# Optimization experiments

Measured on AMD Instinct MI355X. Metric: run time of the kernel, lower is better.

## Reference

```python
import jax, jax.numpy as jnp
import numpy as np

BLKQ = 64
BLKK = 64
TOPK_RATIO = 0.125


def setup_inputs() -> dict:
    key = jax.random.key(0)
    ks = jax.random.split(key, 4)
    B, L, H, D = 1, 4096, 16, 64
    q = jax.random.normal(ks[0], (B, L, H, D), jnp.float32)
    k = jax.random.normal(ks[1], (B, L, H, D), jnp.float32)
    v = jax.random.normal(ks[2], (B, L, H, D), jnp.float32)
    w_proj = jax.random.normal(ks[3], (D, D), jnp.float32) * 0.02
    b_proj = jnp.zeros((D,), jnp.float32)
    return {"q": q, "k": k, "v": v, "w_proj": w_proj, "b_proj": b_proj}


def _sparse_linear_attn(q, k, v, w_proj, b_proj):
    # q,k,v: (B, L, H, D) -> (B, H, L, D)
    q = jnp.transpose(q, (0, 2, 1, 3))
    k = jnp.transpose(k, (0, 2, 1, 3))
    v = jnp.transpose(v, (0, 2, 1, 3))
    B, H, L, D = q.shape
    M, N = L // BLKQ, L // BLKK  # L chosen divisible by block sizes (no padding)
    T = max(1, int(TOPK_RATIO * N))  # selected key blocks per query block

    qb = q.reshape(B, H, M, BLKQ, D)
    kb = k.reshape(B, H, N, BLKK, D)
    vb = v.reshape(B, H, N, BLKK, D)

    # --- block map: mean-pooled block descriptors, topk key blocks per query block ---
    qm = qb.mean(axis=3)  # (B,H,M,D)
    km = kb.mean(axis=3)  # (B,H,N,D)
    blk_scores = jnp.einsum('bhmd,bhnd->bhmn', qm, km)
    _, lut = jax.lax.top_k(blk_scores, T)  # (B,H,M,T) int32

    # --- gather selected K/V blocks ---
    b_idx = jnp.arange(B)[:, None, None, None]
    h_idx = jnp.arange(H)[None, :, None, None]
    k_sel = kb[b_idx, h_idx, lut]  # (B,H,M,T,BLKK,D)
    v_sel = vb[b_idx, h_idx, lut]  # (B,H,M,T,BLKK,D)

    # --- block-sparse softmax attention over gathered keys only ---
    scale = D ** (-0.5)
    att = jnp.einsum('bhmqd,bhmtkd->bhmqtk', qb, k_sel) * scale
    att = att.reshape(B, H, M, BLKQ, T * BLKK)
    p = jax.nn.softmax(att, axis=-1)
    o_s = jnp.einsum('bhmqn,bhmnd->bhmqd', p, v_sel.reshape(B, H, M, T * BLKK, D))
    o_s = o_s.reshape(B, H, L, D)

    # --- global linear attention with softmax feature map ---
    q_fm = jax.nn.softmax(q, axis=-1)
    k_fm = jax.nn.softmax(k, axis=-1)
    kvsum = jnp.einsum('bhld,bhle->bhde', k_fm, v)  # (B,H,D,D)
    ksum = k_fm.sum(axis=2)  # (B,H,D)
    num = jnp.einsum('bhld,bhde->bhle', q_fm, kvsum)
    den = jnp.einsum('bhld,bhd->bhl', q_fm, ksum)[..., None] + 1e-6
    o_l = num / den
    o_l = jnp.einsum('bhld,ed->bhle', o_l, w_proj) + b_proj  # nn.Linear: x @ W.T + b

    o = o_s + o_l
    return jnp.transpose(o, (0, 2, 1, 3))  # (B, L, H, D)


def reference(q, k, v, w_proj, b_proj):
    return _sparse_linear_attn(q, k, v, w_proj, b_proj)
```

## Files before the change

### kernel.cpp

```cpp
#include <hip/hip_runtime.h>


#define NH   16
#define DH   64
#define NBLK 64
#define TSEL 8

typedef unsigned short u16;
typedef unsigned int   u32;
typedef __attribute__((ext_vector_type(8))) short short8;
typedef __attribute__((ext_vector_type(4))) float f4;
typedef __attribute__((ext_vector_type(4))) u32 u32x4;

#define MFMA_BF16(a, b, c) __builtin_amdgcn_mfma_f32_16x16x32_bf16(a, b, c, 0, 0, 0)

__device__ __forceinline__ u16 f2bf_rne(float f) {
  u32 u = __float_as_uint(f);
  u += 0x7fffu + ((u >> 16) & 1u);
  return (u16)(u >> 16);
}
__device__ __forceinline__ u32 pk2(float a, float b) {
  return (u32)f2bf_rne(a) | ((u32)f2bf_rne(b) << 16);
}
__device__ __forceinline__ float bf2f(u16 u) { return __uint_as_float(((u32)u) << 16); }

__device__ __forceinline__ short8 frag_row(const u16* t, int row, int jblk) {
  return *(const short8*)((const char*)t + row * 128 + ((jblk ^ (row & 7)) * 16));
}

__device__ __forceinline__ void gload_lds16(const char* g, char* l) {
  __builtin_amdgcn_global_load_lds(
      (const __attribute__((address_space(1))) char*)g,
      (__attribute__((address_space(3))) char*)l, 16, 0, 0);
}

__device__ __forceinline__ void stage_async(const char* ktb, const char* vtb,
                                            char* dst, int w, int lane) {
  const char* s = ((w & 2) ? vtb : ktb) + (w & 1) * 4096 + lane * 16;
  char* d = dst + ((w & 2) ? 8192 : 0) + (w & 1) * 4096 + lane * 16;
#pragma unroll
  for (int i = 0; i < 4; i++) gload_lds16(s + i * 1024, d + i * 1024);
}

__device__ __forceinline__ void stage_m2(const char* m2b, const float* ksum_h,
                                         const float* bproj, char* dst,
                                         int w, int lane) {
  if (w < 2) {
    const char* s = m2b + w * 4096 + lane * 16;
    char* d = dst + w * 4096 + lane * 16;
#pragma unroll
    for (int i = 0; i < 4; i++) gload_lds16(s + i * 1024, d + i * 1024);
  } else if (w == 2 && lane < 32) {
    const char* s = (lane < 16) ? ((const char*)ksum_h + lane * 16)
                                : ((const char*)bproj + (lane - 16) * 16);
    gload_lds16(s, dst + 8192 + lane * 16);
  }
}

__global__ __launch_bounds__(256) void prep_kernel(const float* __restrict__ k,
                                                   const float* __restrict__ v,
                                                   u16* __restrict__ kT,
                                                   u16* __restrict__ vT,
                                                   float* __restrict__ kvp,
                                                   float* __restrict__ ksp,
                                                   float* __restrict__ kmv) {
  __shared__ __align__(16) char vsl[8192];
  __shared__ __align__(16) char kfm[8192];
  __shared__ float redmx[256];
  __shared__ float redsm[256];
  __shared__ float kmred[256];
  __shared__ float ksred[256];
  __shared__ float mxf[64];
  __shared__ float smi[64];
  int b = blockIdx.x;
  int n = (b >> 3) & 63;
  int h = 2 * (b & 7) + (b >> 9);
  int tid = threadIdx.x;
  int w = tid >> 6, lane = tid & 63;
  int row = lane, qd = w;
  int lq = lane & 15, quad = lane >> 4;

  float kv[16];
  {
    const float* kr = k + (size_t)(n * 64 + row) * 1024 + h * 64 + qd * 16;
#pragma unroll
    for (int c4 = 0; c4 < 4; c4++) {
      float4 a = *(const float4*)(kr + c4 * 4);
      kv[c4 * 4] = a.x; kv[c4 * 4 + 1] = a.y; kv[c4 * 4 + 2] = a.z; kv[c4 * 4 + 3] = a.w;
    }
  }
  {
    uint4 w0 = make_uint4(pk2(kv[0], kv[1]), pk2(kv[2], kv[3]),
                          pk2(kv[4], kv[5]), pk2(kv[6], kv[7]));
    uint4 w1 = make_uint4(pk2(kv[8], kv[9]), pk2(kv[10], kv[11]),
                          pk2(kv[12], kv[13]), pk2(kv[14], kv[15]));
    *(uint4*)(vsl + row * 128 + (((2 * qd) ^ (row & 7)) * 16)) = w0;
    *(uint4*)(vsl + row * 128 + (((2 * qd + 1) ^ (row & 7)) * 16)) = w1;
  }
  {
    float mx = kv[0];
#pragma unroll
    for (int j = 1; j < 16; j++) mx = fmaxf(mx, kv[j]);
    redmx[qd * 64 + row] = mx;
  }
  __syncthreads();

  {
    uint4* kt_out = (uint4*)(kT + ((size_t)(h * 64 + n)) * 4096);
    kt_out[tid] = ((const uint4*)vsl)[tid];
    kt_out[256 + tid] = ((const uint4*)vsl)[256 + tid];
  }
  {
    float mx = fmaxf(fmaxf(redmx[row], redmx[64 + row]),
                     fmaxf(redmx[128 + row], redmx[192 + row]));
    float sm = 0.f;
#pragma unroll
    for (int j = 0; j < 16; j++) sm += __expf(kv[j] - mx);
    redsm[qd * 64 + row] = sm;
  }
  __syncthreads();
  if (tid < 64) {
    mxf[tid] = fmaxf(fmaxf(redmx[tid], redmx[64 + tid]),
                     fmaxf(redmx[128 + tid], redmx[192 + tid]));
    smi[tid] = 1.0f / (redsm[tid] + redsm[64 + tid] + redsm[128 + tid] + redsm[192 + tid]);
  }
  __syncthreads();

  {
    int c = lane, g = w;
    const float* kcg = k + (size_t)(n * 64 + g * 16) * 1024 + h * 64 + c;
    float e[16];
    float pk = 0.f;
#pragma unroll
    for (int i = 0; i < 16; i++) {
      float x = kcg[(size_t)i * 1024];
      pk += x;
      int r = g * 16 + i;
      e[i] = __expf(x - mxf[r]) * smi[r];
    }
    kmred[g * 64 + c] = pk;
    uint4 x0 = make_uint4(pk2(e[0], e[1]), pk2(e[2], e[3]),
                          pk2(e[4], e[5]), pk2(e[6], e[7]));
    uint4 x1 = make_uint4(pk2(e[8], e[9]), pk2(e[10], e[11]),
                          pk2(e[12], e[13]), pk2(e[14], e[15]));
    *(uint4*)(kfm + c * 128 + (((2 * g) ^ (c & 7)) * 16)) = x0;
    *(uint4*)(kfm + c * 128 + (((2 * g + 1) ^ (c & 7)) * 16)) = x1;
  }
  {
    int c = lane, g = w;
    const float* vcol = v + (size_t)(n * 64 + g * 16) * 1024 + h * 64 + c;
    float vv[16];
#pragma unroll
    for (int i = 0; i < 16; i++) vv[i] = vcol[(size_t)i * 1024];
    uint4 x0 = make_uint4(pk2(vv[0], vv[1]), pk2(vv[2], vv[3]),
                          pk2(vv[4], vv[5]), pk2(vv[6], vv[7]));
    uint4 x1 = make_uint4(pk2(vv[8], vv[9]), pk2(vv[10], vv[11]),
                          pk2(vv[12], vv[13]), pk2(vv[14], vv[15]));
    *(uint4*)(vsl + c * 128 + (((2 * g) ^ (c & 7)) * 16)) = x0;
    *(uint4*)(vsl + c * 128 + (((2 * g + 1) ^ (c & 7)) * 16)) = x1;
  }
  __syncthreads();

  {
    uint4* vt_out = (uint4*)(vT + ((size_t)(h * 64 + n)) * 4096);
    vt_out[tid] = ((const uint4*)vsl)[tid];
    vt_out[256 + tid] = ((const uint4*)vsl)[256 + tid];
  }
  if (tid < 64)
    kmv[h * 4096 + n * 64 + tid] =
        (kmred[tid] + kmred[64 + tid] + kmred[128 + tid] + kmred[192 + tid]) * (1.0f / 64.0f);
  {
    float ks = 0.f;
    short8 x0 = frag_row((const u16*)kfm, lane, 2 * w);
    short8 x1 = frag_row((const u16*)kfm, lane, 2 * w + 1);
#pragma unroll
    for (int e = 0; e < 8; e++) ks += bf2f((u16)x0[e]) + bf2f((u16)x1[e]);
    ksred[tid] = ks;
  }
  {
    f4 acc[4];
    f4 zz = {0.f, 0.f, 0.f, 0.f};
#pragma unroll
    for (int et = 0; et < 4; et++) acc[et] = zz;
#pragma unroll
    for (int ks2 = 0; ks2 < 2; ks2++) {
      short8 a_ = frag_row((const u16*)kfm, w * 16 + lq, 4 * ks2 + quad);
#pragma unroll
      for (int et = 0; et < 4; et++)
        acc[et] = MFMA_BF16(a_, frag_row((const u16*)vsl, et * 16 + lq, 4 * ks2 + quad), acc[et]);
    }
    float* kvb = kvp + ((size_t)(h * 64 + n)) * 4096;
#pragma unroll
    for (int r = 0; r < 4; r++)
#pragma unroll
      for (int et = 0; et < 4; et++)
        kvb[(w * 16 + quad * 4 + r) * 64 + et * 16 + lq] = acc[et][r];
  }
  __syncthreads();
  if (tid < 64)
    ksp[((size_t)(h * 64 + n)) * 64 + tid] = ksred[tid] + ksred[64 + tid] +
                                             ksred[128 + tid] + ksred[192 + tid];
}

__global__ __launch_bounds__(256) void post_kernel(const float* __restrict__ kvp,
                                                   const float* __restrict__ ksp,
                                                   const float* __restrict__ wgt,
                                                   u16* __restrict__ m2t,
                                                   float* __restrict__ ksum) {
  __shared__ float kr[4][64];
  __shared__ float wl[64 * 65];
  int bx = blockIdx.x, tid = threadIdx.x;
  int h = bx >> 4, dq = bx & 15;
  int j = tid & 63, rr = tid >> 6;

  {
    size_t off = (size_t)(dq * 4 + rr) * 64 + j;
    const float* base = kvp + (size_t)h * 64 * 4096 + off;
    float s0 = 0.f, s1 = 0.f, s2 = 0.f, s3 = 0.f;
#pragma unroll
    for (int n4 = 0; n4 < 16; n4++) {
      s0 += base[(size_t)(n4 * 4 + 0) * 4096];
      s1 += base[(size_t)(n4 * 4 + 1) * 4096];
      s2 += base[(size_t)(n4 * 4 + 2) * 4096];
      s3 += base[(size_t)(n4 * 4 + 3) * 4096];
    }
    kr[rr][j] = (s0 + s1) + (s2 + s3);
  }
#pragma unroll
  for (int i = 0; i < 16; i++) {
    int f = i * 256 + tid;
    wl[(f >> 6) * 65 + (f & 63)] = wgt[f];
  }
  __syncthreads();

  {
    int e = tid & 63, rr2 = tid >> 6;
    float acc = 0.f;
#pragma unroll
    for (int jj = 0; jj < 64; jj++) acc = fmaf(kr[rr2][jj], wl[e * 65 + jj], acc);
    int d = dq * 4 + rr2;
    *(u16*)((char*)m2t + (size_t)h * 8192 + e * 128 +
            (((d >> 3) ^ (e & 7)) * 16) + (d & 7) * 2) = f2bf_rne(acc);
  }
  if (dq == 0 && tid < 64) {
    const float* base = ksp + (size_t)h * 64 * 64 + tid;
    float s = 0.f;
#pragma unroll
    for (int n = 0; n < 64; n++) s += base[(size_t)n * 64];
    ksum[h * 64 + tid] = s;
  }
}

__global__ __launch_bounds__(256, 4) void fused_attn_kernel(const float* __restrict__ q,
                                                            const u16* __restrict__ kT,
                                                            const u16* __restrict__ vT,
                                                            const float* __restrict__ kmv,
                                                            const u16* __restrict__ m2t,
                                                            const float* __restrict__ ksum,
                                                            const float* __restrict__ bproj,
                                                            float* __restrict__ out) {
  __shared__ __align__(16) char smem[40960];
  int b = blockIdx.x;
  int m = (b >> 3) & 63;
  int h = 2 * (b & 7) + (b >> 9);
  int tid = threadIdx.x, w = tid >> 6, lane = tid & 63;
  int lq = lane & 15, quad = lane >> 4;
  char* bufA = smem;
  char* bufB = smem + 16384;
  char* p_b = smem + 32768 + w * 2048;
  float* km_s = (float*)smem;
  float* qmp = (float*)(smem + 20480);
  float* qmf = (float*)(smem + 21504);

  {
    int c = tid & 63, g = tid >> 6;
    const float* qcol = q + ((size_t)(m * 64 + g * 16)) * 1024 + h * 64 + c;
    float qp = 0.f;
#pragma unroll
    for (int i = 0; i < 16; i++) qp += qcol[(size_t)i * 1024];
    qmp[g * 64 + c] = qp;
#pragma unroll
    for (int i = 0; i < 16; i++) {
      int idx = i * 256 + tid;
      km_s[(idx >> 6) * 65 + (idx & 63)] = kmv[h * 4096 + idx];
    }
  }
  __syncthreads();
  if (tid < 64) qmf[tid] = qmp[tid] + qmp[64 + tid] + qmp[128 + tid] + qmp[192 + tid];
  __syncthreads();
  int blks[8];
  {
    int n = lane;
    float s = 0.f;
#pragma unroll
    for (int d = 0; d < 64; d++) s += qmf[d] * km_s[n * 65 + d];
    float my = s;
#pragma unroll
    for (int t = 0; t < TSEL; t++) {
      float vv = my; int idx = n;
#pragma unroll
      for (int off = 1; off < 64; off <<= 1) {
        float ov = __shfl_xor(vv, off);
        int oi = __shfl_xor(idx, off);
        if (ov > vv || (ov == vv && oi < idx)) { vv = ov; idx = oi; }
      }
      int sel = __builtin_amdgcn_readfirstlane(idx);
      blks[t] = sel;
      if (n == sel) my = -INFINITY;
    }
  }
  __syncthreads();

  const int qrow = w * 16 + lq;
  const float* qr_g = q + ((size_t)(m * 64 + qrow)) * 1024 + h * 64;
  short8 qf[2];
#pragma unroll
  for (int ks = 0; ks < 2; ks++) {
    const float* gp = qr_g + (4 * ks + quad) * 8;
    float4 a = *(const float4*)gp;
    float4 bb = *(const float4*)(gp + 4);
    u32x4 tt = {pk2(a.x, a.y), pk2(a.z, a.w), pk2(bb.x, bb.y), pk2(bb.z, bb.w)};
    qf[ks] = __builtin_bit_cast(short8, tt);
  }

  stage_async((const char*)(kT + ((size_t)(h * 64 + blks[0])) * 4096),
              (const char*)(vT + ((size_t)(h * 64 + blks[0])) * 4096),
              bufA, w, lane);
  __syncthreads();

  float mrun = -INFINITY, lrun = 0.f;
  f4 o[4];
  f4 zz = {0.f, 0.f, 0.f, 0.f};
#pragma unroll
  for (int et = 0; et < 4; et++) o[et] = zz;

  char* cur = bufA;
  char* nxt = bufB;

  for (int t = 0; t < 8; t++) {
    if (t < 7)
      stage_async((const char*)(kT + ((size_t)(h * 64 + blks[t + 1])) * 4096),
                  (const char*)(vT + ((size_t)(h * 64 + blks[t + 1])) * 4096),
                  nxt, w, lane);
    else
      stage_m2((const char*)m2t + (size_t)h * 8192, ksum + h * 64, bproj,
               nxt, w, lane);

    const u16* kc = (const u16*)cur;
    const u16* vc = (const u16*)(cur + 8192);

    f4 s[4];
#pragma unroll
    for (int kt = 0; kt < 4; kt++) s[kt] = zz;
    __builtin_amdgcn_s_setprio(1);
#pragma unroll
    for (int ks = 0; ks < 2; ks++)
#pragma unroll
      for (int kt = 0; kt < 4; kt++)
        s[kt] = MFMA_BF16(frag_row(kc, kt * 16 + lq, 4 * ks + quad), qf[ks], s[kt]);
    __builtin_amdgcn_s_setprio(0);

    float mp = -INFINITY;
#pragma unroll
    for (int kt = 0; kt < 4; kt++)
#pragma unroll
      for (int r = 0; r < 4; r++) mp = fmaxf(mp, s[kt][r]);
    mp = fmaxf(mp, __shfl_xor(mp, 16));
    mp = fmaxf(mp, __shfl_xor(mp, 32));
    mp *= 0.125f;
    if (__any(mp > mrun)) {
      float mn = fmaxf(mrun, mp);
      float al = __expf(mrun - mn);
      mrun = mn;
      lrun *= al;
#pragma unroll
      for (int et = 0; et < 4; et++)
#pragma unroll
        for (int r = 0; r < 4; r++) o[et][r] *= al;
    }
    float rs_ = 0.f;
#pragma unroll
    for (int kt = 0; kt < 4; kt++) {
      float p0 = __expf(fmaf(s[kt][0], 0.125f, -mrun));
      float p1 = __expf(fmaf(s[kt][1], 0.125f, -mrun));
      float p2 = __expf(fmaf(s[kt][2], 0.125f, -mrun));
      float p3 = __expf(fmaf(s[kt][3], 0.125f, -mrun));
      rs_ += p0 + p1 + p2 + p3;
      u32 lo32 = (__float_as_uint(p0) >> 16) | (__float_as_uint(p1) & 0xffff0000u);
      u32 hi32 = (__float_as_uint(p2) >> 16) | (__float_as_uint(p3) & 0xffff0000u);
      int addr = lq * 128 + (((kt * 2 + (quad >> 1)) ^ (lq & 7)) * 16) + (quad & 1) * 8;
      *(uint2*)(p_b + addr) = make_uint2(lo32, hi32);
    }
    rs_ += __shfl_xor(rs_, 16);
    rs_ += __shfl_xor(rs_, 32);
    lrun += rs_;

    __builtin_amdgcn_s_setprio(1);
#pragma unroll
    for (int ks = 0; ks < 2; ks++) {
      short8 pf = frag_row((const u16*)p_b, lq, 4 * ks + quad);
#pragma unroll
      for (int et = 0; et < 4; et++)
        o[et] = MFMA_BF16(frag_row(vc, et * 16 + lq, 4 * ks + quad), pf, o[et]);
    }
    __builtin_amdgcn_s_setprio(0);

    __syncthreads();
    char* tmp = cur; cur = nxt; nxt = tmp;
  }

  u16* m2_l = (u16*)cur;
  float* ks_s = (float*)(cur + 8192);
  float* b_s = (float*)(cur + 8448);

  float ev[16];
  float mx = -INFINITY;
#pragma unroll
  for (int c4 = 0; c4 < 4; c4++) {
    float4 a = *(const float4*)(qr_g + quad * 16 + c4 * 4);
    ev[c4 * 4] = a.x; ev[c4 * 4 + 1] = a.y; ev[c4 * 4 + 2] = a.z; ev[c4 * 4 + 3] = a.w;
    mx = fmaxf(mx, fmaxf(fmaxf(a.x, a.y), fmaxf(a.z, a.w)));
  }
  mx = fmaxf(mx, __shfl_xor(mx, 16));
  mx = fmaxf(mx, __shfl_xor(mx, 32));
  float sum = 0.f, eks = 0.f;
#pragma unroll
  for (int j = 0; j < 16; j++) {
    float e = __expf(ev[j] - mx);
    ev[j] = e;
    sum += e;
    eks += e * ks_s[quad * 16 + j];
  }
  sum += __shfl_xor(sum, 16); sum += __shfl_xor(sum, 32);
  eks += __shfl_xor(eks, 16); eks += __shfl_xor(eks, 32);
  float invs = 1.0f / sum;
  float den = fmaf(eks, invs, 1e-6f);
  float scale = invs / den;
  uint4 e0v = make_uint4(pk2(ev[0], ev[1]), pk2(ev[2], ev[3]),
                         pk2(ev[4], ev[5]), pk2(ev[6], ev[7]));
  uint4 e1v = make_uint4(pk2(ev[8], ev[9]), pk2(ev[10], ev[11]),
                         pk2(ev[12], ev[13]), pk2(ev[14], ev[15]));
  *(uint4*)(p_b + lq * 128 + (((2 * quad) ^ (lq & 7)) * 16)) = e0v;
  *(uint4*)(p_b + lq * 128 + (((2 * quad + 1) ^ (lq & 7)) * 16)) = e1v;

  f4 oc[4];
  f4 zz2 = {0.f, 0.f, 0.f, 0.f};
#pragma unroll
  for (int et = 0; et < 4; et++) oc[et] = zz2;
  __builtin_amdgcn_s_setprio(1);
#pragma unroll
  for (int ks2 = 0; ks2 < 2; ks2++) {
    short8 ef = frag_row((const u16*)p_b, lq, 4 * ks2 + quad);
#pragma unroll
    for (int et = 0; et < 4; et++)
      oc[et] = MFMA_BF16(frag_row(m2_l, et * 16 + lq, 4 * ks2 + quad), ef, oc[et]);
  }
  __builtin_amdgcn_s_setprio(0);

  float invl = 1.0f / lrun;
  float* gp = out + ((size_t)(m * 64 + qrow)) * 1024 + h * 64 + quad * 4;
#pragma unroll
  for (int et = 0; et < 4; et++) {
    int e0 = et * 16 + quad * 4;
    float4 ov;
    ov.x = o[et][0] * invl + oc[et][0] * scale + b_s[e0 + 0];
    ov.y = o[et][1] * invl + oc[et][1] * scale + b_s[e0 + 1];
    ov.z = o[et][2] * invl + oc[et][2] * scale + b_s[e0 + 2];
    ov.w = o[et][3] * invl + oc[et][3] * scale + b_s[e0 + 3];
    *(float4*)(gp + et * 16) = ov;
  }
}

extern "C" void kernel_launch(void* const* d_in, const int* in_sizes, int n_in,
                              void* d_out, int out_size, void* d_ws, size_t ws_size,
                              hipStream_t stream) {
  const float* q = (const float*)d_in[0];
  const float* k = (const float*)d_in[1];
  const float* v = (const float*)d_in[2];
  const float* w = (const float*)d_in[3];
  const float* b = (const float*)d_in[4];
  float* out = (float*)d_out;

  u16* kT = (u16*)d_ws;
  u16* vT = kT + 4194304;
  float* kvp = (float*)(vT + 4194304);
  float* ksp = kvp + 4194304;
  float* kmv = ksp + 65536;
  float* ksum = kmv + 65536;
  u16* m2t = (u16*)(ksum + 1024);

  prep_kernel<<<1024, 256, 0, stream>>>(k, v, kT, vT, kvp, ksp, kmv);
  post_kernel<<<256, 256, 0, stream>>>(kvp, ksp, w, m2t, ksum);
  fused_attn_kernel<<<1024, 256, 0, stream>>>(q, kT, vT, kmv, m2t, ksum, b, out);
}
```

Before: 130.5 us.

## Move block top-k selection out of attention kernel into prep/post kernels

Query block pooling now runs in prep_kernel, and the block score plus top-k selection runs in 16 extra post_kernel blocks, one per head. Each of those blocks handles all 64 query blocks and writes a LUT. Before, every attention block reloaded the full key-mean table for its head (16KB) and ran the selection itself, behind two barriers. The attention kernel now only reads 8 indices from the LUT. In exchange, the top-k work is serialized into 16 blocks that each loop over 16 query blocks per wave, which may lengthen post_kernel.

```diff
diff --git a/kernel.cpp b/kernel.cpp
--- a/kernel.cpp
+++ b/kernel.cpp
@@ -57,19 +57,22 @@
   }
 }
 
-__global__ __launch_bounds__(256) void prep_kernel(const float* __restrict__ k,
+__global__ __launch_bounds__(256) void prep_kernel(const float* __restrict__ q,
+                                                   const float* __restrict__ k,
                                                    const float* __restrict__ v,
                                                    u16* __restrict__ kT,
                                                    u16* __restrict__ vT,
                                                    float* __restrict__ kvp,
                                                    float* __restrict__ ksp,
-                                                   float* __restrict__ kmv) {
+                                                   float* __restrict__ kmv,
+                                                   float* __restrict__ qm) {
   __shared__ __align__(16) char vsl[8192];
   __shared__ __align__(16) char kfm[8192];
   __shared__ float redmx[256];
   __shared__ float redsm[256];
   __shared__ float kmred[256];
   __shared__ float ksred[256];
+  __shared__ float qred[256];
   __shared__ float mxf[64];
   __shared__ float smi[64];
   int b = blockIdx.x;
@@ -159,6 +162,14 @@
     *(uint4*)(vsl + c * 128 + (((2 * g) ^ (c & 7)) * 16)) = x0;
     *(uint4*)(vsl + c * 128 + (((2 * g + 1) ^ (c & 7)) * 16)) = x1;
   }
+  {
+    int c = lane, g = w;
+    const float* qcol = q + (size_t)(n * 64 + g * 16) * 1024 + h * 64 + c;
+    float qp = 0.f;
+#pragma unroll
+    for (int i = 0; i < 16; i++) qp += qcol[(size_t)i * 1024];
+    qred[g * 64 + c] = qp;
+  }
   __syncthreads();
 
   {
@@ -166,9 +177,12 @@
     vt_out[tid] = ((const uint4*)vsl)[tid];
     vt_out[256 + tid] = ((const uint4*)vsl)[256 + tid];
   }
-  if (tid < 64)
+  if (tid < 64) {
     kmv[h * 4096 + n * 64 + tid] =
         (kmred[tid] + kmred[64 + tid] + kmred[128 + tid] + kmred[192 + tid]) * (1.0f / 64.0f);
+    qm[h * 4096 + n * 64 + tid] =
+        qred[tid] + qred[64 + tid] + qred[128 + tid] + qred[192 + tid];
+  }
   {
     float ks = 0.f;
     short8 x0 = frag_row((const u16*)kfm, lane, 2 * w);
@@ -205,59 +219,96 @@
 __global__ __launch_bounds__(256) void post_kernel(const float* __restrict__ kvp,
                                                    const float* __restrict__ ksp,
                                                    const float* __restrict__ wgt,
+                                                   const float* __restrict__ qm,
+                                                   const float* __restrict__ kmv,
                                                    u16* __restrict__ m2t,
-                                                   float* __restrict__ ksum) {
-  __shared__ float kr[4][64];
-  __shared__ float wl[64 * 65];
+                                                   float* __restrict__ ksum,
+                                                   int* __restrict__ lut) {
+  __shared__ __align__(16) char pmem[33280];
   int bx = blockIdx.x, tid = threadIdx.x;
-  int h = bx >> 4, dq = bx & 15;
-  int j = tid & 63, rr = tid >> 6;
-
-  {
-    size_t off = (size_t)(dq * 4 + rr) * 64 + j;
-    const float* base = kvp + (size_t)h * 64 * 4096 + off;
-    float s0 = 0.f, s1 = 0.f, s2 = 0.f, s3 = 0.f;
-#pragma unroll
-    for (int n4 = 0; n4 < 16; n4++) {
-      s0 += base[(size_t)(n4 * 4 + 0) * 4096];
-      s1 += base[(size_t)(n4 * 4 + 1) * 4096];
-      s2 += base[(size_t)(n4 * 4 + 2) * 4096];
-      s3 += base[(size_t)(n4 * 4 + 3) * 4096];
-    }
-    kr[rr][j] = (s0 + s1) + (s2 + s3);
-  }
-#pragma unroll
-  for (int i = 0; i < 16; i++) {
-    int f = i * 256 + tid;
-    wl[(f >> 6) * 65 + (f & 63)] = wgt[f];
-  }
-  __syncthreads();
-
-  {
-    int e = tid & 63, rr2 = tid >> 6;
-    float acc = 0.f;
-#pragma unroll
-    for (int jj = 0; jj < 64; jj++) acc = fmaf(kr[rr2][jj], wl[e * 65 + jj], acc);
-    int d = dq * 4 + rr2;
-    *(u16*)((char*)m2t + (size_t)h * 8192 + e * 128 +
-            (((d >> 3) ^ (e & 7)) * 16) + (d & 7) * 2) = f2bf_rne(acc);
-  }
-  if (dq == 0 && tid < 64) {
-    const float* base = ksp + (size_t)h * 64 * 64 + tid;
-    float s = 0.f;
-#pragma unroll
-    for (int n = 0; n < 64; n++) s += base[(size_t)n * 64];
-    ksum[h * 64 + tid] = s;
+  if (bx < 256) {
+    float* kr = (float*)pmem;
+    float* wl = (float*)(pmem + 1024);
+    int h = bx >> 4, dq = bx & 15;
+    int j = tid & 63, rr = tid >> 6;
+    {
+      size_t off = (size_t)(dq * 4 + rr) * 64 + j;
+      const float* base = kvp + (size_t)h * 64 * 4096 + off;
+      float s0 = 0.f, s1 = 0.f, s2 = 0.f, s3 = 0.f;
+#pragma unroll
+      for (int n4 = 0; n4 < 16; n4++) {
+        s0 += base[(size_t)(n4 * 4 + 0) * 4096];
+        s1 += base[(size_t)(n4 * 4 + 1) * 4096];
+        s2 += base[(size_t)(n4 * 4 + 2) * 4096];
+        s3 += base[(size_t)(n4 * 4 + 3) * 4096];
+      }
+      kr[rr * 64 + j] = (s0 + s1) + (s2 + s3);
+    }
+#pragma unroll
+    for (int i = 0; i < 16; i++) {
+      int f = i * 256 + tid;
+      wl[(f >> 6) * 65 + (f & 63)] = wgt[f];
+    }
+    __syncthreads();
+    {
+      int e = tid & 63, rr2 = tid >> 6;
+      float acc = 0.f;
+#pragma unroll
+      for (int jj = 0; jj < 64; jj++) acc = fmaf(kr[rr2 * 64 + jj], wl[e * 65 + jj], acc);
+      int d = dq * 4 + rr2;
+      *(u16*)((char*)m2t + (size_t)h * 8192 + e * 128 +
+              (((d >> 3) ^ (e & 7)) * 16) + (d & 7) * 2) = f2bf_rne(acc);
+    }
+    if (dq == 0 && tid < 64) {
+      const float* base = ksp + (size_t)h * 64 * 64 + tid;
+      float s = 0.f;
+#pragma unroll
+      for (int n = 0; n < 64; n++) s += base[(size_t)n * 64];
+      ksum[h * 64 + tid] = s;
+    }
+  } else {
+    float* qm_s = (float*)pmem;
+    float* km_l = (float*)(pmem + 16640);
+    int h = bx - 256;
+    int w = tid >> 6, lane = tid & 63;
+#pragma unroll
+    for (int i = 0; i < 16; i++) {
+      int idx = i * 256 + tid;
+      qm_s[(idx >> 6) * 65 + (idx & 63)] = qm[h * 4096 + idx];
+      km_l[(idx >> 6) * 65 + (idx & 63)] = kmv[h * 4096 + idx];
+    }
+    __syncthreads();
+    int n = lane;
+    for (int j = 0; j < 16; j++) {
+      int m = j * 4 + w;
+      float s = 0.f;
+#pragma unroll
+      for (int d = 0; d < 64; d++) s += qm_s[m * 65 + d] * km_l[n * 65 + d];
+      float my = s;
+#pragma unroll
+      for (int t = 0; t < TSEL; t++) {
+        float vv = my; int idx = n;
+#pragma unroll
+        for (int off = 1; off < 64; off <<= 1) {
+          float ov = __shfl_xor(vv, off);
+          int oi = __shfl_xor(idx, off);
+          if (ov > vv || (ov == vv && oi < idx)) { vv = ov; idx = oi; }
+        }
+        int sel = __builtin_amdgcn_readfirstlane(idx);
+        if (n == 0) lut[(h * 64 + m) * TSEL + t] = sel;
+        if (n == sel) my = -INFINITY;
+      }
+    }
   }
 }
 
 __global__ __launch_bounds__(256, 4) void fused_attn_kernel(const float* __restrict__ q,
                                                             const u16* __restrict__ kT,
                                                             const u16* __restrict__ vT,
-                                                            const float* __restrict__ kmv,
                                                             const u16* __restrict__ m2t,
                                                             const float* __restrict__ ksum,
                                                             const float* __restrict__ bproj,
+                                                            const int* __restrict__ lut,
                                                             float* __restrict__ out) {
   __shared__ __align__(16) char smem[40960];
   int b = blockIdx.x;
@@ -268,48 +319,13 @@
   char* bufA = smem;
   char* bufB = smem + 16384;
   char* p_b = smem + 32768 + w * 2048;
-  float* km_s = (float*)smem;
-  float* qmp = (float*)(smem + 20480);
-  float* qmf = (float*)(smem + 21504);
-
-  {
-    int c = tid & 63, g = tid >> 6;
-    const float* qcol = q + ((size_t)(m * 64 + g * 16)) * 1024 + h * 64 + c;
-    float qp = 0.f;
-#pragma unroll
-    for (int i = 0; i < 16; i++) qp += qcol[(size_t)i * 1024];
-    qmp[g * 64 + c] = qp;
-#pragma unroll
-    for (int i = 0; i < 16; i++) {
-      int idx = i * 256 + tid;
-      km_s[(idx >> 6) * 65 + (idx & 63)] = kmv[h * 4096 + idx];
-    }
-  }
-  __syncthreads();
-  if (tid < 64) qmf[tid] = qmp[tid] + qmp[64 + tid] + qmp[128 + tid] + qmp[192 + tid];
-  __syncthreads();
+
   int blks[8];
   {
-    int n = lane;
-    float s = 0.f;
-#pragma unroll
-    for (int d = 0; d < 64; d++) s += qmf[d] * km_s[n * 65 + d];
-    float my = s;
-#pragma unroll
-    for (int t = 0; t < TSEL; t++) {
-      float vv = my; int idx = n;
-#pragma unroll
-      for (int off = 1; off < 64; off <<= 1) {
-        float ov = __shfl_xor(vv, off);
-        int oi = __shfl_xor(idx, off);
-        if (ov > vv || (ov == vv && oi < idx)) { vv = ov; idx = oi; }
-      }
-      int sel = __builtin_amdgcn_readfirstlane(idx);
-      blks[t] = sel;
-      if (n == sel) my = -INFINITY;
-    }
-  }
-  __syncthreads();
+    const int* lp = lut + (h * 64 + m) * TSEL;
+#pragma unroll
+    for (int t = 0; t < 8; t++) blks[t] = lp[t];
+  }
 
   const int qrow = w * 16 + lq;
   const float* qr_g = q + ((size_t)(m * 64 + qrow)) * 1024 + h * 64;
@@ -488,8 +504,10 @@
   float* kmv = ksp + 65536;
   float* ksum = kmv + 65536;
   u16* m2t = (u16*)(ksum + 1024);
-
-  prep_kernel<<<1024, 256, 0, stream>>>(k, v, kT, vT, kvp, ksp, kmv);
-  post_kernel<<<256, 256, 0, stream>>>(kvp, ksp, w, m2t, ksum);
-  fused_attn_kernel<<<1024, 256, 0, stream>>>(q, kT, vT, kmv, m2t, ksum, b, out);
-}
+  float* qm = (float*)(m2t + 65536);
+  int* lut = (int*)(qm + 65536);
+
+  prep_kernel<<<1024, 256, 0, stream>>>(q, k, v, kT, vT, kvp, ksp, kmv, qm);
+  post_kernel<<<272, 256, 0, stream>>>(kvp, ksp, w, qm, kmv, m2t, ksum, lut);
+  fused_attn_kernel<<<1024, 256, 0, stream>>>(q, kT, vT, m2t, ksum, b, lut, out);
+}
```

Result: slower. 199.7 us (+53.0%).
